# Kernel tuning notes

Hardware: AMD Instinct MI355X
Metric: run time of the kernel (lower is better)

## Reference

```python
import jax, jax.numpy as jnp
import numpy as np

CLAMP = 10.0  # forward default arg `clamp`


def setup_inputs() -> dict:
    key = jax.random.key(0)
    k1, k2, k3, k4 = jax.random.split(key, 4)
    B, N = 256, 8192
    return {
        "pred_frames": jax.random.normal(k1, (B, N, 4, 4), dtype=jnp.float32),
        "true_frames": jax.random.normal(k2, (B, N, 4, 4), dtype=jnp.float32),
        "pred_pos": jax.random.normal(k3, (B, N, 3), dtype=jnp.float32),
        "true_pos": jax.random.normal(k4, (B, N, 3), dtype=jnp.float32),
    }


def reference(pred_frames, true_frames, pred_pos, true_pos):
    # Batched Kabsch alignment of pred_pos -> true_pos, then clamped point error.
    # pred_frames / true_frames are unused by the original module's forward.
    cA = pred_pos.mean(axis=1, keepdims=True)  # [B,1,3]
    cB = true_pos.mean(axis=1, keepdims=True)  # [B,1,3]
    AA = pred_pos - cA                          # [B,N,3]
    BB = true_pos - cB                          # [B,N,3]
    H = jnp.einsum('bni,bnj->bij', AA, BB)      # [B,3,3] covariance
    U, S, Vt = jnp.linalg.svd(H)
    # R = Vt^T @ U^T : R[b,i,k] = sum_j Vt[b,j,i] * U[b,k,j]
    R = jnp.einsum('bji,bkj->bik', Vt, U)
    det = jnp.linalg.det(R)                     # [B]
    sign = jnp.where(det < 0, -1.0, 1.0).astype(Vt.dtype)
    Vt_fixed = Vt.at[:, -1, :].multiply(sign[:, None])  # flip last row if det<0
    R = jnp.einsum('bji,bkj->bik', Vt_fixed, U)
    # t = centroid_B - R @ centroid_A (vector of shape [B,3])
    t = cB[:, 0, :] - jnp.einsum('bij,bj->bi', R, cA[:, 0, :])
    # NOTE: original applies pred_pos @ R (not R^T) + t, replicated faithfully.
    pred_aligned = jnp.einsum('bni,bij->bnj', pred_pos, R) + t[:, None, :]
    dist = jnp.linalg.norm(pred_aligned - true_pos, axis=-1)  # [B,N]
    # clamp(max=CLAMP).mean() per batch, then averaged over batch == global mean
    return jnp.mean(jnp.minimum(dist, CLAMP))
```

## Files before the change

### kernel.cpp

```cpp
#include <hip/hip_runtime.h>
#include <math.h>

#define NB 256
#define NPT 8192
#define SPLITS 4
#define CHUNK (NPT / SPLITS)
#define THREADS 256
#define CLAMPV 10.0f

__global__ __launch_bounds__(THREADS) void cov_kernel(
    const float* __restrict__ pred, const float* __restrict__ tru,
    float* __restrict__ stats)
{
    const int blk = blockIdx.x;
    const int b  = blk >> 2;
    const int sp = blk & 3;
    const float* P = pred + ((size_t)b * NPT + (size_t)sp * CHUNK) * 3;
    const float* T = tru  + ((size_t)b * NPT + (size_t)sp * CHUNK) * 3;

    float acc[15];
#pragma unroll
    for (int i = 0; i < 15; ++i) acc[i] = 0.f;

    for (int n = threadIdx.x; n < CHUNK; n += THREADS) {
        const float px = P[3*n+0], py = P[3*n+1], pz = P[3*n+2];
        const float tx = T[3*n+0], ty = T[3*n+1], tz = T[3*n+2];
        acc[0] += px; acc[1] += py; acc[2] += pz;
        acc[3] += tx; acc[4] += ty; acc[5] += tz;
        acc[6]  += px*tx; acc[7]  += px*ty; acc[8]  += px*tz;
        acc[9]  += py*tx; acc[10] += py*ty; acc[11] += py*tz;
        acc[12] += pz*tx; acc[13] += pz*ty; acc[14] += pz*tz;
    }
#pragma unroll
    for (int i = 0; i < 15; ++i)
        for (int off = 32; off > 0; off >>= 1)
            acc[i] += __shfl_down(acc[i], off, 64);

    __shared__ float smem[THREADS/64][15];
    const int wave = threadIdx.x >> 6, lane = threadIdx.x & 63;
    if (lane == 0) {
#pragma unroll
        for (int i = 0; i < 15; ++i) smem[wave][i] = acc[i];
    }
    __syncthreads();
    if (threadIdx.x < 15) {
        float s = 0.f;
#pragma unroll
        for (int w = 0; w < THREADS/64; ++w) s += smem[w][threadIdx.x];
        stats[(size_t)blk * 16 + threadIdx.x] = s;
    }
}

__device__ inline double det3(const double m[3][3]) {
    return m[0][0]*(m[1][1]*m[2][2]-m[1][2]*m[2][1])
         - m[0][1]*(m[1][0]*m[2][2]-m[1][2]*m[2][0])
         + m[0][2]*(m[1][0]*m[2][1]-m[1][1]*m[2][0]);
}

__global__ void svd_kernel(const float* __restrict__ stats, float* __restrict__ RT)
{
    const int b = blockIdx.x * blockDim.x + threadIdx.x;
    if (b >= NB) return;

    double sA[3] = {0,0,0}, sB[3] = {0,0,0}, M[9] = {0,0,0,0,0,0,0,0,0};
    for (int sp = 0; sp < SPLITS; ++sp) {
        const float* st = stats + ((size_t)(b * SPLITS + sp)) * 16;
        for (int i = 0; i < 3; ++i) sA[i] += st[i];
        for (int i = 0; i < 3; ++i) sB[i] += st[3 + i];
        for (int i = 0; i < 9; ++i) M[i]  += st[6 + i];
    }
    double cA[3], cB[3];
    for (int i = 0; i < 3; ++i) { cA[i] = sA[i] / NPT; cB[i] = sB[i] / NPT; }

    double H[3][3];
    for (int i = 0; i < 3; ++i)
        for (int j = 0; j < 3; ++j)
            H[i][j] = M[i*3 + j] - (double)NPT * cA[i] * cB[j];

    double A[3][3];
    for (int i = 0; i < 3; ++i)
        for (int j = 0; j < 3; ++j) {
            double s = 0.0;
            for (int k = 0; k < 3; ++k) s += H[k][i] * H[k][j];
            A[i][j] = s;
        }
    double V[3][3] = {{1,0,0},{0,1,0},{0,0,1}};
    const int PQ[3][2] = {{0,1},{0,2},{1,2}};
    for (int sweep = 0; sweep < 15; ++sweep) {
        for (int r = 0; r < 3; ++r) {
            const int p = PQ[r][0], q = PQ[r][1];
            const double apq = A[p][q];
            if (fabs(apq) < 1e-300) continue;
            const double theta = (A[q][q] - A[p][p]) / (2.0 * apq);
            const double t = copysign(1.0, theta) / (fabs(theta) + sqrt(theta*theta + 1.0));
            const double c = 1.0 / sqrt(t*t + 1.0);
            const double s = t * c;
            for (int k = 0; k < 3; ++k) {
                const double akp = A[k][p], akq = A[k][q];
                A[k][p] = c*akp - s*akq;
                A[k][q] = s*akp + c*akq;
            }
            for (int k = 0; k < 3; ++k) {
                const double apk = A[p][k], aqk = A[q][k];
                A[p][k] = c*apk - s*aqk;
                A[q][k] = s*apk + c*aqk;
            }
            for (int k = 0; k < 3; ++k) {
                const double vkp = V[k][p], vkq = V[k][q];
                V[k][p] = c*vkp - s*vkq;
                V[k][q] = s*vkp + c*vkq;
            }
        }
    }
    double eig[3] = {A[0][0], A[1][1], A[2][2]};
    int idx[3] = {0, 1, 2};
    if (eig[idx[0]] < eig[idx[1]]) { int t_ = idx[0]; idx[0] = idx[1]; idx[1] = t_; }
    if (eig[idx[0]] < eig[idx[2]]) { int t_ = idx[0]; idx[0] = idx[2]; idx[2] = t_; }
    if (eig[idx[1]] < eig[idx[2]]) { int t_ = idx[1]; idx[1] = idx[2]; idx[2] = t_; }

    double Vc[3][3], Uc[3][3];
    for (int i = 0; i < 3; ++i) {
        const int j = idx[i];
        for (int r = 0; r < 3; ++r) Vc[r][i] = V[r][j];
    }
    for (int i = 0; i < 3; ++i) {
        double u[3];
        for (int r = 0; r < 3; ++r)
            u[r] = H[r][0]*Vc[0][i] + H[r][1]*Vc[1][i] + H[r][2]*Vc[2][i];
        const double nrm = sqrt(u[0]*u[0] + u[1]*u[1] + u[2]*u[2]);
        if (nrm > 1e-30) {
            for (int r = 0; r < 3; ++r) Uc[r][i] = u[r] / nrm;
        } else if (i == 2) {
            Uc[0][2] = Uc[1][0]*Uc[2][1] - Uc[2][0]*Uc[1][1];
            Uc[1][2] = Uc[2][0]*Uc[0][1] - Uc[0][0]*Uc[2][1];
            Uc[2][2] = Uc[0][0]*Uc[1][1] - Uc[1][0]*Uc[0][1];
        } else {
            for (int r = 0; r < 3; ++r) Uc[r][i] = (r == i) ? 1.0 : 0.0;
        }
    }
    if (det3(Uc) * det3(Vc) < 0.0)
        for (int r = 0; r < 3; ++r) Vc[r][2] = -Vc[r][2];

    double R[3][3];
    for (int i = 0; i < 3; ++i)
        for (int k = 0; k < 3; ++k)
            R[i][k] = Vc[i][0]*Uc[k][0] + Vc[i][1]*Uc[k][1] + Vc[i][2]*Uc[k][2];
    double tv[3];
    for (int i = 0; i < 3; ++i)
        tv[i] = cB[i] - (R[i][0]*cA[0] + R[i][1]*cA[1] + R[i][2]*cA[2]);

    float* o = RT + (size_t)b * 12;
    for (int i = 0; i < 3; ++i)
        for (int j = 0; j < 3; ++j)
            o[i*3 + j] = (float)R[i][j];
    for (int i = 0; i < 3; ++i) o[9 + i] = (float)tv[i];
}

__global__ __launch_bounds__(THREADS) void dist_kernel(
    const float* __restrict__ pred, const float* __restrict__ tru,
    const float* __restrict__ RT, float* __restrict__ partial)
{
    const int blk = blockIdx.x;
    const int b  = blk >> 2;
    const int sp = blk & 3;
    const float* P = pred + ((size_t)b * NPT + (size_t)sp * CHUNK) * 3;
    const float* T = tru  + ((size_t)b * NPT + (size_t)sp * CHUNK) * 3;
    const float* rt = RT + (size_t)b * 12;
    const float R00 = rt[0], R01 = rt[1], R02 = rt[2];
    const float R10 = rt[3], R11 = rt[4], R12 = rt[5];
    const float R20 = rt[6], R21 = rt[7], R22 = rt[8];
    const float t0 = rt[9], t1 = rt[10], t2 = rt[11];

    float acc = 0.f;
    for (int n = threadIdx.x; n < CHUNK; n += THREADS) {
        const float px = P[3*n+0], py = P[3*n+1], pz = P[3*n+2];
        const float tx = T[3*n+0], ty = T[3*n+1], tz = T[3*n+2];
        const float ax = px*R00 + py*R10 + pz*R20 + t0;
        const float ay = px*R01 + py*R11 + pz*R21 + t1;
        const float az = px*R02 + py*R12 + pz*R22 + t2;
        const float dx = ax - tx, dy = ay - ty, dz = az - tz;
        const float d = sqrtf(dx*dx + dy*dy + dz*dz);
        acc += fminf(d, CLAMPV);
    }
    for (int off = 32; off > 0; off >>= 1)
        acc += __shfl_down(acc, off, 64);
    __shared__ float smem[THREADS/64];
    const int wave = threadIdx.x >> 6, lane = threadIdx.x & 63;
    if (lane == 0) smem[wave] = acc;
    __syncthreads();
    if (threadIdx.x == 0) {
        float s = 0.f;
#pragma unroll
        for (int w = 0; w < THREADS/64; ++w) s += smem[w];
        partial[blk] = s;
    }
}

__global__ __launch_bounds__(THREADS) void finalize_kernel(
    const float* __restrict__ partial, float* __restrict__ out)
{
    float acc = 0.f;
    for (int i = threadIdx.x; i < NB * SPLITS; i += THREADS) acc += partial[i];
    for (int off = 32; off > 0; off >>= 1)
        acc += __shfl_down(acc, off, 64);
    __shared__ float smem[THREADS/64];
    const int wave = threadIdx.x >> 6, lane = threadIdx.x & 63;
    if (lane == 0) smem[wave] = acc;
    __syncthreads();
    if (threadIdx.x == 0) {
        float s = 0.f;
#pragma unroll
        for (int w = 0; w < THREADS/64; ++w) s += smem[w];
        out[0] = s / 2097152.0f;
    }
}

extern "C" void kernel_launch(void* const* d_in, const int* in_sizes, int n_in,
                              void* d_out, int out_size, void* d_ws, size_t ws_size,
                              hipStream_t stream)
{
    const float* pred_pos = (const float*)d_in[2];
    const float* true_pos = (const float*)d_in[3];
    float* out = (float*)d_out;

    float* ws      = (float*)d_ws;
    float* stats   = ws;
    float* RT      = ws + (size_t)NB * SPLITS * 16;
    float* partial = RT + (size_t)NB * 12;

    cov_kernel<<<NB * SPLITS, THREADS, 0, stream>>>(pred_pos, true_pos, stats);
    svd_kernel<<<1, NB, 0, stream>>>(stats, RT);
    dist_kernel<<<NB * SPLITS, THREADS, 0, stream>>>(pred_pos, true_pos, RT, partial);
    finalize_kernel<<<1, THREADS, 0, stream>>>(partial, out);
}
```

Measured before the change: 273.4 us.

## Vectorize point loads with float4, cut Jacobi sweeps, fold finalize into atomics

Both streaming kernels now load four points per thread as three float4 vectors from each array instead of scalar strided loads, which widens memory transactions. The Jacobi eigen-solver drops from 15 to 6 sweeps. The separate finalize kernel is removed: the SVD kernel zeroes the output and each dist block atomically adds its scaled partial sum. This saves a launch but makes the float summation order nondeterministic, and fewer sweeps could reduce eigenvector accuracy for ill-conditioned covariance matrices.

```diff
diff --git a/kernel.cpp b/kernel.cpp
--- a/kernel.cpp
+++ b/kernel.cpp
@@ -7,6 +7,7 @@
 #define CHUNK (NPT / SPLITS)
 #define THREADS 256
 #define CLAMPV 10.0f
+#define INV_TOTAL (1.0f / 2097152.0f)
 
 __global__ __launch_bounds__(THREADS) void cov_kernel(
     const float* __restrict__ pred, const float* __restrict__ tru,
@@ -22,14 +23,25 @@
 #pragma unroll
     for (int i = 0; i < 15; ++i) acc[i] = 0.f;
 
-    for (int n = threadIdx.x; n < CHUNK; n += THREADS) {
-        const float px = P[3*n+0], py = P[3*n+1], pz = P[3*n+2];
-        const float tx = T[3*n+0], ty = T[3*n+1], tz = T[3*n+2];
-        acc[0] += px; acc[1] += py; acc[2] += pz;
-        acc[3] += tx; acc[4] += ty; acc[5] += tz;
-        acc[6]  += px*tx; acc[7]  += px*ty; acc[8]  += px*tz;
-        acc[9]  += py*tx; acc[10] += py*ty; acc[11] += py*tz;
-        acc[12] += pz*tx; acc[13] += pz*ty; acc[14] += pz*tz;
+    for (int n0 = threadIdx.x * 4; n0 < CHUNK; n0 += THREADS * 4) {
+        const float4* Pq = (const float4*)(P + 3 * n0);
+        const float4* Tq = (const float4*)(T + 3 * n0);
+        const float4 pa = Pq[0], pb = Pq[1], pc = Pq[2];
+        const float4 ta = Tq[0], tb = Tq[1], tc = Tq[2];
+        const float px[4] = {pa.x, pa.w, pb.z, pc.y};
+        const float py[4] = {pa.y, pb.x, pb.w, pc.z};
+        const float pz[4] = {pa.z, pb.y, pc.x, pc.w};
+        const float tx[4] = {ta.x, ta.w, tb.z, tc.y};
+        const float ty[4] = {ta.y, tb.x, tb.w, tc.z};
+        const float tz[4] = {ta.z, tb.y, tc.x, tc.w};
+#pragma unroll
+        for (int k = 0; k < 4; ++k) {
+            acc[0] += px[k]; acc[1] += py[k]; acc[2] += pz[k];
+            acc[3] += tx[k]; acc[4] += ty[k]; acc[5] += tz[k];
+            acc[6]  += px[k]*tx[k]; acc[7]  += px[k]*ty[k]; acc[8]  += px[k]*tz[k];
+            acc[9]  += py[k]*tx[k]; acc[10] += py[k]*ty[k]; acc[11] += py[k]*tz[k];
+            acc[12] += pz[k]*tx[k]; acc[13] += pz[k]*ty[k]; acc[14] += pz[k]*tz[k];
+        }
     }
 #pragma unroll
     for (int i = 0; i < 15; ++i)
@@ -57,9 +69,11 @@
          + m[0][2]*(m[1][0]*m[2][1]-m[1][1]*m[2][0]);
 }
 
-__global__ void svd_kernel(const float* __restrict__ stats, float* __restrict__ RT)
+__global__ void svd_kernel(const float* __restrict__ stats, float* __restrict__ RT,
+                           float* __restrict__ out)
 {
     const int b = blockIdx.x * blockDim.x + threadIdx.x;
+    if (b == 0) out[0] = 0.f;
     if (b >= NB) return;
 
     double sA[3] = {0,0,0}, sB[3] = {0,0,0}, M[9] = {0,0,0,0,0,0,0,0,0};
@@ -86,7 +100,7 @@
         }
     double V[3][3] = {{1,0,0},{0,1,0},{0,0,1}};
     const int PQ[3][2] = {{0,1},{0,2},{1,2}};
-    for (int sweep = 0; sweep < 15; ++sweep) {
+    for (int sweep = 0; sweep < 6; ++sweep) {
         for (int r = 0; r < 3; ++r) {
             const int p = PQ[r][0], q = PQ[r][1];
             const double apq = A[p][q];
@@ -158,7 +172,7 @@
 
 __global__ __launch_bounds__(THREADS) void dist_kernel(
     const float* __restrict__ pred, const float* __restrict__ tru,
-    const float* __restrict__ RT, float* __restrict__ partial)
+    const float* __restrict__ RT, float* __restrict__ out)
 {
     const int blk = blockIdx.x;
     const int b  = blk >> 2;
@@ -172,15 +186,26 @@
     const float t0 = rt[9], t1 = rt[10], t2 = rt[11];
 
     float acc = 0.f;
-    for (int n = threadIdx.x; n < CHUNK; n += THREADS) {
-        const float px = P[3*n+0], py = P[3*n+1], pz = P[3*n+2];
-        const float tx = T[3*n+0], ty = T[3*n+1], tz = T[3*n+2];
-        const float ax = px*R00 + py*R10 + pz*R20 + t0;
-        const float ay = px*R01 + py*R11 + pz*R21 + t1;
-        const float az = px*R02 + py*R12 + pz*R22 + t2;
-        const float dx = ax - tx, dy = ay - ty, dz = az - tz;
-        const float d = sqrtf(dx*dx + dy*dy + dz*dz);
-        acc += fminf(d, CLAMPV);
+    for (int n0 = threadIdx.x * 4; n0 < CHUNK; n0 += THREADS * 4) {
+        const float4* Pq = (const float4*)(P + 3 * n0);
+        const float4* Tq = (const float4*)(T + 3 * n0);
+        const float4 pa = Pq[0], pb = Pq[1], pc = Pq[2];
+        const float4 ta = Tq[0], tb = Tq[1], tc = Tq[2];
+        const float px[4] = {pa.x, pa.w, pb.z, pc.y};
+        const float py[4] = {pa.y, pb.x, pb.w, pc.z};
+        const float pz[4] = {pa.z, pb.y, pc.x, pc.w};
+        const float tx[4] = {ta.x, ta.w, tb.z, tc.y};
+        const float ty[4] = {ta.y, tb.x, tb.w, tc.z};
+        const float tz[4] = {ta.z, tb.y, tc.x, tc.w};
+#pragma unroll
+        for (int k = 0; k < 4; ++k) {
+            const float ax = px[k]*R00 + py[k]*R10 + pz[k]*R20 + t0;
+            const float ay = px[k]*R01 + py[k]*R11 + pz[k]*R21 + t1;
+            const float az = px[k]*R02 + py[k]*R12 + pz[k]*R22 + t2;
+            const float dx = ax - tx[k], dy = ay - ty[k], dz = az - tz[k];
+            const float d = sqrtf(dx*dx + dy*dy + dz*dz);
+            acc += fminf(d, CLAMPV);
+        }
     }
     for (int off = 32; off > 0; off >>= 1)
         acc += __shfl_down(acc, off, 64);
@@ -192,26 +217,7 @@
         float s = 0.f;
 #pragma unroll
         for (int w = 0; w < THREADS/64; ++w) s += smem[w];
-        partial[blk] = s;
-    }
-}
-
-__global__ __launch_bounds__(THREADS) void finalize_kernel(
-    const float* __restrict__ partial, float* __restrict__ out)
-{
-    float acc = 0.f;
-    for (int i = threadIdx.x; i < NB * SPLITS; i += THREADS) acc += partial[i];
-    for (int off = 32; off > 0; off >>= 1)
-        acc += __shfl_down(acc, off, 64);
-    __shared__ float smem[THREADS/64];
-    const int wave = threadIdx.x >> 6, lane = threadIdx.x & 63;
-    if (lane == 0) smem[wave] = acc;
-    __syncthreads();
-    if (threadIdx.x == 0) {
-        float s = 0.f;
-#pragma unroll
-        for (int w = 0; w < THREADS/64; ++w) s += smem[w];
-        out[0] = s / 2097152.0f;
+        atomicAdd(out, s * INV_TOTAL);
     }
 }
 
@@ -223,13 +229,11 @@
     const float* true_pos = (const float*)d_in[3];
     float* out = (float*)d_out;
 
-    float* ws      = (float*)d_ws;
-    float* stats   = ws;
-    float* RT      = ws + (size_t)NB * SPLITS * 16;
-    float* partial = RT + (size_t)NB * 12;
+    float* ws    = (float*)d_ws;
+    float* stats = ws;
+    float* RT    = ws + (size_t)NB * SPLITS * 16;
 
     cov_kernel<<<NB * SPLITS, THREADS, 0, stream>>>(pred_pos, true_pos, stats);
-    svd_kernel<<<1, NB, 0, stream>>>(stats, RT);
-    dist_kernel<<<NB * SPLITS, THREADS, 0, stream>>>(pred_pos, true_pos, RT, partial);
-    finalize_kernel<<<1, THREADS, 0, stream>>>(partial, out);
-}
+    svd_kernel<<<1, NB, 0, stream>>>(stats, RT, out);
+    dist_kernel<<<NB * SPLITS, THREADS, 0, stream>>>(pred_pos, true_pos, RT, out);
+}
```

Result: no change. 276.0 us (+0.9%).
